# Kernel tuning notes

Measured on AMD Instinct MI355X. Metric: run time of the kernel, lower is better.

## Reference

```python
import jax, jax.numpy as jnp
import numpy as np

B, T, C = 4, 1024, 1024
H = 16
DH = C // H  # 64


def setup_inputs() -> dict:
    key = jax.random.key(0)
    ks = jax.random.split(key, 10)
    s = 0.02
    return {
        "x": jax.random.normal(ks[0], (B, T, C), dtype=jnp.float32),
        "Wq": jax.random.normal(ks[1], (C, C), dtype=jnp.float32) * s,
        "bq": jnp.zeros((C,), dtype=jnp.float32),
        "Wk": jax.random.normal(ks[2], (C, C), dtype=jnp.float32) * s,
        "bk": jnp.zeros((C,), dtype=jnp.float32),
        "Wv": jax.random.normal(ks[3], (C, C), dtype=jnp.float32) * s,
        "bv": jnp.zeros((C,), dtype=jnp.float32),
        "Wp": jax.random.normal(ks[4], (C, C), dtype=jnp.float32) * s,
        "bp": jnp.zeros((C,), dtype=jnp.float32),
    }


def reference(x, Wq, bq, Wk, bk, Wv, bv, Wp, bp):
    b, t, c = x.shape
    # QKV projections, split into heads: [b, H, t, DH]
    def heads(y):
        return y.reshape(b, t, H, DH).transpose(0, 2, 1, 3)
    q = heads(x @ Wq + bq)
    k = heads(x @ Wk + bk)
    v = heads(x @ Wv + bv)
    # Causal attention. Original masks with -inf BEFORE scaling; -inf*scale is
    # still -inf, so mask-then-scale == scale-then-mask.
    scores = jnp.einsum("bhqd,bhkd->bhqk", q, k) * (DH ** -0.5)
    causal = jnp.tril(jnp.ones((t, t), dtype=bool))
    scores = jnp.where(causal, scores, -jnp.inf)
    attn = jax.nn.softmax(scores, axis=-1)  # dropout p=0.0 -> identity
    ctx = jnp.einsum("bhqk,bhkd->bhqd", attn, v)
    ctx = ctx.transpose(0, 2, 1, 3).reshape(b, t, c)
    return ctx @ Wp + bp
```

## Files before the change

### kernel.cpp

```cpp
#include <hip/hip_runtime.h>


typedef unsigned short ushort_t;
typedef __attribute__((ext_vector_type(8))) __bf16 bf16x8;
typedef __attribute__((ext_vector_type(8))) unsigned short us8;
typedef __attribute__((ext_vector_type(4))) unsigned short us4;
typedef __attribute__((ext_vector_type(4))) float f32x4;

#define AS1 __attribute__((address_space(1)))
#define AS3 __attribute__((address_space(3)))

__device__ __forceinline__ ushort_t f2bf(float f) {
  unsigned int u = __float_as_uint(f);
  u += 0x7fffu + ((u >> 16) & 1u);
  return (ushort_t)(u >> 16);
}


__global__ void cvt_x_kernel(const float* __restrict__ x, ushort_t* __restrict__ xb) {
  const int i = blockIdx.x * 256 + threadIdx.x;
  const float4 v = reinterpret_cast<const float4*>(x)[i];
  us4 o;
  o.x = f2bf(v.x); o.y = f2bf(v.y); o.z = f2bf(v.z); o.w = f2bf(v.w);
  reinterpret_cast<us4*>(xb)[i] = o;
}

__global__ void cvt_w4_kernel(const float* __restrict__ Wq, const float* __restrict__ Wk,
                              const float* __restrict__ Wv, const float* __restrict__ Wp,
                              ushort_t* __restrict__ WQKVT, ushort_t* __restrict__ WPT) {
  __shared__ float t[32][33];
  const int z = blockIdx.z;
  const float* W = (z == 0) ? Wq : (z == 1) ? Wk : (z == 2) ? Wv : Wp;
  ushort_t* Wt = (z == 3) ? WPT : (WQKVT + ((size_t)z << 20));
  const float wscale = (z == 0) ? 0.125f : 1.0f;
  const int n0 = blockIdx.x * 32, k0 = blockIdx.y * 32;
  const int tx = threadIdx.x, ty = threadIdx.y;
#pragma unroll
  for (int i = ty; i < 32; i += 8)
    t[i][tx] = W[(size_t)(k0 + i) * 1024 + n0 + tx];
  __syncthreads();
#pragma unroll
  for (int i = ty; i < 32; i += 8)
    Wt[(size_t)(n0 + i) * 1024 + k0 + tx] = f2bf(t[tx][i] * wscale);
}

__global__ void vtrans_kernel(const ushort_t* __restrict__ QKV, ushort_t* __restrict__ VT) {
  const int x = blockIdx.x;
  const int bh = blockIdx.y;
  const int b = bh >> 4, h = bh & 15;
  __shared__ ushort_t L[64 * 72];
  const int tid = threadIdx.x;
#pragma unroll
  for (int it = 0; it < 2; ++it) {
    const int c = it * 256 + tid;
    const int tr = c >> 3, dd = (c & 7) << 3;
    *reinterpret_cast<us8*>(&L[tr * 72 + dd]) = *reinterpret_cast<const us8*>(
        QKV + ((size_t)b * 1024 + x * 64 + tr) * 3072 + 2048 + h * 64 + dd);
  }
  __syncthreads();
#pragma unroll
  for (int it = 0; it < 2; ++it) {
    const int c = it * 256 + tid;
    const int dr = c >> 3, tt = (c & 7) << 3;
    us8 o;
#pragma unroll
    for (int e = 0; e < 8; ++e) o[e] = L[(tt + e) * 72 + dr];
    *reinterpret_cast<us8*>(VT + ((size_t)bh * 64 + dr) * 1024 + x * 64 + tt) = o;
  }
}


template <int BM, int OUT_BF16>
__global__ __launch_bounds__(256, 2) void gemm_bt_kernel(
    const ushort_t* __restrict__ A, const ushort_t* __restrict__ Bt,
    const float* __restrict__ b0, const float* __restrict__ b1,
    const float* __restrict__ b2, void* __restrict__ Cout,
    int N, int K, int nbx, float bscale0) {
  constexpr int WR = BM / 2;
  constexpr int MFR = BM / 32;
  constexpr int NIT = (BM + 128) / 64;
  __shared__ ushort_t As[BM * 32];
  __shared__ ushort_t Bs[128 * 32];
  const int tid = threadIdx.x;
  const int wave = tid >> 6, lane = tid & 63;
  const int lgrp = lane >> 4, lmod = lane & 15;
  const int wr = wave >> 1, wc = wave & 1;
  const int cpx = gridDim.x >> 3;
  const int swz = (blockIdx.x & 7) * cpx + (blockIdx.x >> 3);
  const int row0 = (swz / nbx) * BM, col0 = (swz % nbx) * 128;

  f32x4 acc[MFR][4] = {};

  for (int k0 = 0; k0 < K; k0 += 32) {
#pragma unroll
    for (int it = 0; it < NIT; ++it) {
      const int c0 = it * 256 + wave * 64;
      const int c = c0 + lane;
      if (c0 < BM * 4) {
        const int r = c >> 2, kk = (c & 3) << 3;
        __builtin_amdgcn_global_load_lds(
            (AS1 void*)(A + (size_t)(row0 + r) * K + k0 + kk),
            (AS3 void*)(As + (c0 << 3)), 16, 0, 0);
      } else {
        const int cb = c - BM * 4;
        const int r = cb >> 2, kk = (cb & 3) << 3;
        __builtin_amdgcn_global_load_lds(
            (AS1 void*)(Bt + (size_t)(col0 + r) * K + k0 + kk),
            (AS3 void*)(Bs + ((c0 - BM * 4) << 3)), 16, 0, 0);
      }
    }
    __syncthreads();

    bf16x8 af[MFR], bfr[4];
#pragma unroll
    for (int i = 0; i < MFR; ++i)
      af[i] = *reinterpret_cast<const bf16x8*>(&As[(wr * WR + i * 16 + lmod) * 32 + lgrp * 8]);
#pragma unroll
    for (int i = 0; i < 4; ++i)
      bfr[i] = *reinterpret_cast<const bf16x8*>(&Bs[(wc * 64 + i * 16 + lmod) * 32 + lgrp * 8]);
    __builtin_amdgcn_s_setprio(1);
#pragma unroll
    for (int mi = 0; mi < MFR; ++mi)
#pragma unroll
      for (int ni = 0; ni < 4; ++ni)
        acc[mi][ni] = __builtin_amdgcn_mfma_f32_16x16x32_bf16(af[mi], bfr[ni], acc[mi][ni], 0, 0, 0);
    __builtin_amdgcn_s_setprio(0);
    __syncthreads();
  }

  const float* bsel = (col0 < 1024) ? b0 : (col0 < 2048 ? b1 : b2);
  const float bsc = (col0 < 1024) ? bscale0 : 1.0f;
  const int cb0 = col0 & 1023;
  float bvv[4];
#pragma unroll
  for (int ni = 0; ni < 4; ++ni) bvv[ni] = bsel[cb0 + wc * 64 + ni * 16 + lmod] * bsc;
#pragma unroll
  for (int mi = 0; mi < MFR; ++mi) {
#pragma unroll
    for (int ni = 0; ni < 4; ++ni) {
      const int col = col0 + wc * 64 + ni * 16 + lmod;
#pragma unroll
      for (int r = 0; r < 4; ++r) {
        const int row = row0 + wr * WR + mi * 16 + lgrp * 4 + r;
        const float v = acc[mi][ni][r] + bvv[ni];
        if (OUT_BF16)
          ((ushort_t*)Cout)[(size_t)row * N + col] = f2bf(v);
        else
          ((float*)Cout)[(size_t)row * N + col] = v;
      }
    }
  }
}


__global__ __launch_bounds__(256, 2) void attn_kernel(
    const ushort_t* __restrict__ QKV, const ushort_t* __restrict__ VT,
    ushort_t* __restrict__ Og) {
  const int bid = blockIdx.x;
  const int swz = (bid & 7) * 64 + (bid >> 3);
  const int p = swz & 7, bh = swz >> 3;
  const int b = bh >> 4, h = bh & 15;
  const int jmax = 15 - p;
  const int tid = threadIdx.x;
  const int wave = tid >> 6, lane = tid & 63;
  const int lgrp = lane >> 4, lmod = lane & 15;

  __shared__ ushort_t Ks[64 * 72];
  __shared__ ushort_t Vs[64 * 72];
  __shared__ ushort_t Ps[4][16 * 72];

  const size_t xrow0 = (size_t)b * 1024;
  const int qlo = p * 64 + wave * 16;
  const int qhi = jmax * 64 + wave * 16;

  bf16x8 qfl[2], qfh[2];
#pragma unroll
  for (int ks = 0; ks < 2; ++ks) {
    qfl[ks] = *reinterpret_cast<const bf16x8*>(
        QKV + (xrow0 + qlo + lmod) * 3072 + h * 64 + ks * 32 + lgrp * 8);
    qfh[ks] = *reinterpret_cast<const bf16x8*>(
        QKV + (xrow0 + qhi + lmod) * 3072 + h * 64 + ks * 32 + lgrp * 8);
  }

  f32x4 ol[4] = {}, oh[4] = {};
  float ll[4] = {0.f, 0.f, 0.f, 0.f}, lh[4] = {0.f, 0.f, 0.f, 0.f};

  const int sr = tid >> 3;
  const int scc = (tid & 7) << 3;
  us8 kreg0, kreg1, vreg0, vreg1;

  auto load_tile = [&](int j) {
    const ushort_t* kp = QKV + (xrow0 + j * 64 + sr) * 3072 + 1024 + h * 64 + scc;
    kreg0 = *reinterpret_cast<const us8*>(kp);
    kreg1 = *reinterpret_cast<const us8*>(kp + 32 * 3072);
    const ushort_t* vp = VT + ((size_t)bh * 64 + sr) * 1024 + j * 64 + scc;
    vreg0 = *reinterpret_cast<const us8*>(vp);
    vreg1 = *reinterpret_cast<const us8*>(vp + 32 * 1024);
  };
  auto write_tile = [&]() {
    *reinterpret_cast<us8*>(&Ks[sr * 72 + scc]) = kreg0;
    *reinterpret_cast<us8*>(&Ks[(32 + sr) * 72 + scc]) = kreg1;
    *reinterpret_cast<us8*>(&Vs[sr * 72 + scc]) = vreg0;
    *reinterpret_cast<us8*>(&Vs[(32 + sr) * 72 + scc]) = vreg1;
  };

  auto step = [&](const bf16x8* qf, f32x4* oacc, float* lsum, bool diag) {
    f32x4 s[4];
    __builtin_amdgcn_s_setprio(1);
#pragma unroll
    for (int cg = 0; cg < 4; ++cg) {
      f32x4 a = {};
#pragma unroll
      for (int ks = 0; ks < 2; ++ks) {
        bf16x8 kf = *reinterpret_cast<const bf16x8*>(
            &Ks[(cg * 16 + lmod) * 72 + ks * 32 + lgrp * 8]);
        a = __builtin_amdgcn_mfma_f32_16x16x32_bf16(qf[ks], kf, a, 0, 0, 0);
      }
      s[cg] = a;
    }
    __builtin_amdgcn_s_setprio(0);
    if (diag) {
      const int qloc = wave * 16 + lgrp * 4;
#pragma unroll
      for (int cg = 0; cg < 4; ++cg) {
        const int kcol = cg * 16 + lmod;
#pragma unroll
        for (int r = 0; r < 4; ++r)
          if (kcol > qloc + r) s[cg][r] = -1e30f;
      }
    }
#pragma unroll
    for (int cg = 0; cg < 4; ++cg)
#pragma unroll
      for (int r = 0; r < 4; ++r) s[cg][r] = __expf(s[cg][r]);
#pragma unroll
    for (int r = 0; r < 4; ++r)
      lsum[r] += (s[0][r] + s[1][r]) + (s[2][r] + s[3][r]);
#pragma unroll
    for (int cg = 0; cg < 4; ++cg)
#pragma unroll
      for (int r = 0; r < 4; ++r)
        Ps[wave][(lgrp * 4 + r) * 72 + cg * 16 + lmod] = f2bf(s[cg][r]);
    __builtin_amdgcn_s_setprio(1);
#pragma unroll
    for (int ks = 0; ks < 2; ++ks) {
      bf16x8 pf = *reinterpret_cast<const bf16x8*>(
          &Ps[wave][lmod * 72 + ks * 32 + lgrp * 8]);
#pragma unroll
      for (int dhg = 0; dhg < 4; ++dhg) {
        bf16x8 vf = *reinterpret_cast<const bf16x8*>(
            &Vs[(dhg * 16 + lmod) * 72 + ks * 32 + lgrp * 8]);
        oacc[dhg] = __builtin_amdgcn_mfma_f32_16x16x32_bf16(pf, vf, oacc[dhg], 0, 0, 0);
      }
    }
    __builtin_amdgcn_s_setprio(0);
  };

  load_tile(0);
  for (int j = 0; j <= jmax; ++j) {
    __syncthreads();
    write_tile();
    __syncthreads();
    if (j < jmax) load_tile(j + 1);
    if (j <= p) step(qfl, ol, ll, j == p);
    step(qfh, oh, lh, j == jmax);
  }

#pragma unroll
  for (int m = 1; m <= 8; m <<= 1)
#pragma unroll
    for (int r = 0; r < 4; ++r) {
      ll[r] += __shfl_xor(ll[r], m);
      lh[r] += __shfl_xor(lh[r], m);
    }

#pragma unroll
  for (int dhg = 0; dhg < 4; ++dhg) {
    const int col = h * 64 + dhg * 16 + lmod;
#pragma unroll
    for (int r = 0; r < 4; ++r) {
      Og[(xrow0 + qlo + lgrp * 4 + r) * 1024 + col] = f2bf(ol[dhg][r] / ll[r]);
      Og[(xrow0 + qhi + lgrp * 4 + r) * 1024 + col] = f2bf(oh[dhg][r] / lh[r]);
    }
  }
}


extern "C" void kernel_launch(void* const* d_in, const int* in_sizes, int n_in,
                              void* d_out, int out_size, void* d_ws, size_t ws_size,
                              hipStream_t stream) {
  const float* x  = (const float*)d_in[0];
  const float* Wq = (const float*)d_in[1];
  const float* bq = (const float*)d_in[2];
  const float* Wk = (const float*)d_in[3];
  const float* bk = (const float*)d_in[4];
  const float* Wv = (const float*)d_in[5];
  const float* bv = (const float*)d_in[6];
  const float* Wp = (const float*)d_in[7];
  const float* bp = (const float*)d_in[8];
  float* out = (float*)d_out;

  char* ws = (char*)d_ws;
  ushort_t* XB    = (ushort_t*)(ws);
  ushort_t* WQKVT = (ushort_t*)(ws + ( 8ull << 20));
  ushort_t* WPT   = (ushort_t*)(ws + (14ull << 20));
  ushort_t* QKVB  = (ushort_t*)(ws + (16ull << 20));
  ushort_t* VT    = (ushort_t*)(ws + (40ull << 20));

  cvt_x_kernel<<<4096, 256, 0, stream>>>(x, XB);
  cvt_w4_kernel<<<dim3(32, 32, 4), dim3(32, 8), 0, stream>>>(Wq, Wk, Wv, Wp, WQKVT, WPT);
  gemm_bt_kernel<128, 1><<<768, 256, 0, stream>>>(XB, WQKVT, bq, bk, bv, QKVB, 3072, 1024, 24, 0.125f);
  vtrans_kernel<<<dim3(16, 64), 256, 0, stream>>>(QKVB, VT);
  attn_kernel<<<512, 256, 0, stream>>>(QKVB, VT, XB);
  gemm_bt_kernel<64, 0><<<512, 256, 0, stream>>>(XB, WPT, bp, bp, bp, out, 1024, 1024, 8, 1.0f);
}
```

Measured before the change: 99.38 us.

## Replace QKV GEMM with double-buffered 256x256 tile kernel, fuse V transpose

Replaces the 128x128 QKV projection GEMM with a 512-thread, 256x256-tile kernel. It double-buffers LDS with asynchronous global-to-LDS loads and explicit waitcnt and barriers, so the next K-slice load overlaps MFMA work. The V columns are written straight into the transposed VT layout in the epilogue, which removes the separate vtrans kernel launch and its extra round trip through global memory. The tradeoffs are a grid of only 192 blocks, which may underfill the GPU's compute units, higher register and LDS pressure, and strided VT stores.

```diff
diff --git a/kernel.cpp b/kernel.cpp
--- a/kernel.cpp
+++ b/kernel.cpp
@@ -44,41 +44,134 @@
     Wt[(size_t)(n0 + i) * 1024 + k0 + tx] = f2bf(t[tx][i] * wscale);
 }
 
-__global__ void vtrans_kernel(const ushort_t* __restrict__ QKV, ushort_t* __restrict__ VT) {
-  const int x = blockIdx.x;
-  const int bh = blockIdx.y;
-  const int b = bh >> 4, h = bh & 15;
-  __shared__ ushort_t L[64 * 72];
+
+__global__ __launch_bounds__(512, 2) void gemm_qkv256_kernel(
+    const ushort_t* __restrict__ A, const ushort_t* __restrict__ Bt,
+    const float* __restrict__ bq, const float* __restrict__ bk,
+    const float* __restrict__ bv, ushort_t* __restrict__ QKVB,
+    ushort_t* __restrict__ VT) {
+  __shared__ ushort_t smem[2][2][256 * 32];
   const int tid = threadIdx.x;
-#pragma unroll
-  for (int it = 0; it < 2; ++it) {
-    const int c = it * 256 + tid;
-    const int tr = c >> 3, dd = (c & 7) << 3;
-    *reinterpret_cast<us8*>(&L[tr * 72 + dd]) = *reinterpret_cast<const us8*>(
-        QKV + ((size_t)b * 1024 + x * 64 + tr) * 3072 + 2048 + h * 64 + dd);
-  }
-  __syncthreads();
-#pragma unroll
-  for (int it = 0; it < 2; ++it) {
-    const int c = it * 256 + tid;
-    const int dr = c >> 3, tt = (c & 7) << 3;
-    us8 o;
-#pragma unroll
-    for (int e = 0; e < 8; ++e) o[e] = L[(tt + e) * 72 + dr];
-    *reinterpret_cast<us8*>(VT + ((size_t)bh * 64 + dr) * 1024 + x * 64 + tt) = o;
-  }
-}
-
-
-template <int BM, int OUT_BF16>
-__global__ __launch_bounds__(256, 2) void gemm_bt_kernel(
+  const int wave = tid >> 6, lane = tid & 63;
+  const int lgrp = lane >> 4, lmod = lane & 15;
+  const int wr = wave >> 2, wc = wave & 3;
+  const int swz = (blockIdx.x & 7) * 24 + (blockIdx.x >> 3);
+  const int row0 = (swz / 12) * 256, col0 = (swz % 12) * 256;
+
+  const ushort_t* Ag = A + (size_t)row0 * 1024;
+  const ushort_t* Bg = Bt + (size_t)col0 * 1024;
+
+  auto stage8k = [&](ushort_t* reg, const ushort_t* g0, int i) {
+    const int row = i * 128 + wave * 16 + (lane >> 2);
+    const int cb = (lane & 3) << 4;
+    __builtin_amdgcn_global_load_lds(
+        (AS1 void*)(g0 + (size_t)row * 1024 + (cb >> 1)),
+        (AS3 void*)((char*)reg + i * 8192 + wave * 1024), 16, 0, 0);
+  };
+
+  f32x4 acc[8][4] = {};
+  constexpr int nt = 32;
+
+  stage8k(&smem[0][0][0], Ag, 0);
+  stage8k(&smem[0][0][0], Ag, 1);
+  stage8k(&smem[0][1][0], Bg, 0);
+  stage8k(&smem[0][1][0], Bg, 1);
+
+  for (int t = 0; t < nt; ++t) {
+    const int cur = t & 1, nxt = cur ^ 1;
+    const char* curA = (const char*)&smem[cur][0][0];
+    const char* curB = (const char*)&smem[cur][1][0];
+    if (t + 1 < nt) {
+      stage8k(&smem[nxt][0][0], Ag + (t + 1) * 32, 0);
+      stage8k(&smem[nxt][0][0], Ag + (t + 1) * 32, 1);
+      asm volatile("s_waitcnt vmcnt(2)" ::: "memory");
+    } else {
+      asm volatile("s_waitcnt vmcnt(0)" ::: "memory");
+    }
+    __builtin_amdgcn_sched_barrier(0);
+    __builtin_amdgcn_s_barrier();
+
+    bf16x8 bfr[4], af[4];
+#pragma unroll
+    for (int ni = 0; ni < 4; ++ni)
+      bfr[ni] = *reinterpret_cast<const bf16x8*>(
+          curB + (wc * 64 + ni * 16 + lmod) * 64 + lgrp * 16);
+#pragma unroll
+    for (int mi = 0; mi < 4; ++mi)
+      af[mi] = *reinterpret_cast<const bf16x8*>(
+          curA + (wr * 128 + mi * 16 + lmod) * 64 + lgrp * 16);
+    if (t + 1 < nt) {
+      stage8k(&smem[nxt][1][0], Bg + (t + 1) * 32, 0);
+      stage8k(&smem[nxt][1][0], Bg + (t + 1) * 32, 1);
+    }
+    __builtin_amdgcn_s_setprio(1);
+#pragma unroll
+    for (int mi = 0; mi < 4; ++mi)
+#pragma unroll
+      for (int ni = 0; ni < 4; ++ni)
+        acc[mi][ni] = __builtin_amdgcn_mfma_f32_16x16x32_bf16(af[mi], bfr[ni], acc[mi][ni], 0, 0, 0);
+    __builtin_amdgcn_s_setprio(0);
+    __builtin_amdgcn_s_barrier();
+
+#pragma unroll
+    for (int mi = 0; mi < 4; ++mi)
+      af[mi] = *reinterpret_cast<const bf16x8*>(
+          curA + (wr * 128 + (4 + mi) * 16 + lmod) * 64 + lgrp * 16);
+    __builtin_amdgcn_s_setprio(1);
+#pragma unroll
+    for (int mi = 0; mi < 4; ++mi)
+#pragma unroll
+      for (int ni = 0; ni < 4; ++ni)
+        acc[4 + mi][ni] = __builtin_amdgcn_mfma_f32_16x16x32_bf16(af[mi], bfr[ni], acc[4 + mi][ni], 0, 0, 0);
+    __builtin_amdgcn_s_setprio(0);
+    __builtin_amdgcn_s_barrier();
+  }
+
+  if (col0 < 2048) {
+    const float* bsel = (col0 < 1024) ? bq : bk;
+    const float bsc = (col0 < 1024) ? 0.125f : 1.0f;
+    float bvv[4];
+#pragma unroll
+    for (int ni = 0; ni < 4; ++ni)
+      bvv[ni] = bsel[(col0 & 1023) + wc * 64 + ni * 16 + lmod] * bsc;
+#pragma unroll
+    for (int mi = 0; mi < 8; ++mi) {
+#pragma unroll
+      for (int ni = 0; ni < 4; ++ni) {
+        const int col = col0 + wc * 64 + ni * 16 + lmod;
+#pragma unroll
+        for (int r = 0; r < 4; ++r) {
+          const int row = row0 + wr * 128 + mi * 16 + lgrp * 4 + r;
+          QKVB[(size_t)row * 3072 + col] = f2bf(acc[mi][ni][r] + bvv[ni]);
+        }
+      }
+    }
+  } else {
+    float bvv[4];
+#pragma unroll
+    for (int ni = 0; ni < 4; ++ni)
+      bvv[ni] = bv[(col0 - 2048) + wc * 64 + ni * 16 + lmod];
+#pragma unroll
+    for (int mi = 0; mi < 8; ++mi) {
+#pragma unroll
+      for (int ni = 0; ni < 4; ++ni) {
+        const int hd = (col0 - 2048) + wc * 64 + ni * 16 + lmod;
+        const int R = row0 + wr * 128 + mi * 16 + lgrp * 4;
+        const int bb = R >> 10, tl = R & 1023;
+        us4 o;
+#pragma unroll
+        for (int r = 0; r < 4; ++r) o[r] = f2bf(acc[mi][ni][r] + bvv[ni]);
+        *reinterpret_cast<us4*>(VT + ((size_t)(bb * 16 + (hd >> 6)) * 64 + (hd & 63)) * 1024 + tl) = o;
+      }
+    }
+  }
+}
+
+
+__global__ __launch_bounds__(256, 2) void gemm_proj_kernel(
     const ushort_t* __restrict__ A, const ushort_t* __restrict__ Bt,
-    const float* __restrict__ b0, const float* __restrict__ b1,
-    const float* __restrict__ b2, void* __restrict__ Cout,
-    int N, int K, int nbx, float bscale0) {
-  constexpr int WR = BM / 2;
-  constexpr int MFR = BM / 32;
-  constexpr int NIT = (BM + 128) / 64;
+    const float* __restrict__ bias, float* __restrict__ Cout) {
+  constexpr int BM = 64, WR = 32, MFR = 2, NIT = 3;
   __shared__ ushort_t As[BM * 32];
   __shared__ ushort_t Bs[128 * 32];
   const int tid = threadIdx.x;
@@ -87,11 +180,11 @@
   const int wr = wave >> 1, wc = wave & 1;
   const int cpx = gridDim.x >> 3;
   const int swz = (blockIdx.x & 7) * cpx + (blockIdx.x >> 3);
-  const int row0 = (swz / nbx) * BM, col0 = (swz % nbx) * 128;
+  const int row0 = (swz / 8) * BM, col0 = (swz % 8) * 128;
 
   f32x4 acc[MFR][4] = {};
 
-  for (int k0 = 0; k0 < K; k0 += 32) {
+  for (int k0 = 0; k0 < 1024; k0 += 32) {
 #pragma unroll
     for (int it = 0; it < NIT; ++it) {
       const int c0 = it * 256 + wave * 64;
@@ -99,13 +192,13 @@
       if (c0 < BM * 4) {
         const int r = c >> 2, kk = (c & 3) << 3;
         __builtin_amdgcn_global_load_lds(
-            (AS1 void*)(A + (size_t)(row0 + r) * K + k0 + kk),
+            (AS1 void*)(A + (size_t)(row0 + r) * 1024 + k0 + kk),
             (AS3 void*)(As + (c0 << 3)), 16, 0, 0);
       } else {
         const int cb = c - BM * 4;
         const int r = cb >> 2, kk = (cb & 3) << 3;
         __builtin_amdgcn_global_load_lds(
-            (AS1 void*)(Bt + (size_t)(col0 + r) * K + k0 + kk),
+            (AS1 void*)(Bt + (size_t)(col0 + r) * 1024 + k0 + kk),
             (AS3 void*)(Bs + ((c0 - BM * 4) << 3)), 16, 0, 0);
       }
     }
@@ -128,28 +221,20 @@
     __syncthreads();
   }
 
-  const float* bsel = (col0 < 1024) ? b0 : (col0 < 2048 ? b1 : b2);
-  const float bsc = (col0 < 1024) ? bscale0 : 1.0f;
-  const int cb0 = col0 & 1023;
   float bvv[4];
 #pragma unroll
-  for (int ni = 0; ni < 4; ++ni) bvv[ni] = bsel[cb0 + wc * 64 + ni * 16 + lmod] * bsc;
-#pragma unroll
-  for (int mi = 0; mi < MFR; ++mi) {
+  for (int ni = 0; ni < 4; ++ni) bvv[ni] = bias[col0 + wc * 64 + ni * 16 + lmod];
+#pragma unroll
+  for (int mi = 0; mi < MFR; ++mi)
 #pragma unroll
     for (int ni = 0; ni < 4; ++ni) {
       const int col = col0 + wc * 64 + ni * 16 + lmod;
 #pragma unroll
       for (int r = 0; r < 4; ++r) {
         const int row = row0 + wr * WR + mi * 16 + lgrp * 4 + r;
-        const float v = acc[mi][ni][r] + bvv[ni];
-        if (OUT_BF16)
-          ((ushort_t*)Cout)[(size_t)row * N + col] = f2bf(v);
-        else
-          ((float*)Cout)[(size_t)row * N + col] = v;
-      }
-    }
-  }
+        Cout[(size_t)row * 1024 + col] = acc[mi][ni][r] + bvv[ni];
+      }
+    }
 }
 
 
@@ -309,8 +394,7 @@
 
   cvt_x_kernel<<<4096, 256, 0, stream>>>(x, XB);
   cvt_w4_kernel<<<dim3(32, 32, 4), dim3(32, 8), 0, stream>>>(Wq, Wk, Wv, Wp, WQKVT, WPT);
-  gemm_bt_kernel<128, 1><<<768, 256, 0, stream>>>(XB, WQKVT, bq, bk, bv, QKVB, 3072, 1024, 24, 0.125f);
-  vtrans_kernel<<<dim3(16, 64), 256, 0, stream>>>(QKVB, VT);
+  gemm_qkv256_kernel<<<192, 512, 0, stream>>>(XB, WQKVT, bq, bk, bv, QKVB, VT);
   attn_kernel<<<512, 256, 0, stream>>>(QKVB, VT, XB);
-  gemm_bt_kernel<64, 0><<<512, 256, 0, stream>>>(XB, WPT, bp, bp, bp, out, 1024, 1024, 8, 1.0f);
-}
+  gemm_proj_kernel<<<512, 256, 0, stream>>>(XB, WPT, bp, out);
+}
```

New measurement: 98.40 us. Within noise of the previous version (-1.0%).
